# Performance work log

Hardware: AMD Instinct MI355X
Metric: run time of the kernel (lower is better)

The kernel has to match this reference:

```python
import jax, jax.numpy as jnp
import numpy as np

B, H, SEQLEN, HEAD_DIM = 1, 16, 4096, 64
SCALE = 1.0 / float(np.sqrt(HEAD_DIM))


def setup_inputs() -> dict:
    key = jax.random.key(0)
    kq, kk, kv = jax.random.split(key, 3)
    q = jax.random.normal(kq, (B, H, SEQLEN, HEAD_DIM), dtype=jnp.float32)
    k = jax.random.normal(kk, (B, H, HEAD_DIM, SEQLEN), dtype=jnp.float32)  # pre-transposed
    v = jax.random.normal(kv, (B, H, SEQLEN, HEAD_DIM), dtype=jnp.float32)
    return {"q": q, "k": k, "v": v}


def reference(q, k, v):
    # causal additive mask: -inf strictly above the diagonal
    mask = jnp.where(
        jnp.triu(jnp.ones((SEQLEN, SEQLEN), dtype=bool), k=1),
        jnp.float32(-jnp.inf), jnp.float32(0.0),
    ).astype(q.dtype)
    scores = jnp.einsum('bhsd,bhdt->bhst', q, k) * SCALE + mask  # [B,H,S,S]
    row_max = jnp.max(scores, axis=-1, keepdims=True)
    p_exp = jnp.exp(scores - row_max)
    denom = jnp.sum(p_exp, axis=-1, keepdims=True)
    p = p_exp / denom                                            # softmax probs
    out = jnp.einsum('bhst,bhtd->bhsd', p, v)                    # [B,H,S,D]
    row_sum = jnp.sum(p, axis=2)                                 # per-key accumulated attention [B,H,S]
    return (out, row_sum)
```

## Files before the change

kernel.cpp:

```cpp
#include <hip/hip_runtime.h>
#include <hip/hip_bf16.h>

#define HEADS 16
#define SEQ   4096
#define DIM   64
#define QT    64
#define KT    64
#define SCALE 0.125f
#define CF    0.18033688011112042f
#define LOG2E 1.4426950408889634f

typedef __bf16 v8bf  __attribute__((ext_vector_type(8)));
typedef __bf16 v4bf  __attribute__((ext_vector_type(4)));
typedef float  f32x4 __attribute__((ext_vector_type(4)));

__device__ __forceinline__ __bf16 to_bf(float f) { return (__bf16)f; }
__device__ __forceinline__ float ex2(float x) { return __builtin_amdgcn_exp2f(x); }
__device__ __forceinline__ float lg2(float x) { return __builtin_amdgcn_logf(x); }

__device__ __forceinline__ void gload16(const __bf16* g, __bf16* l) {
    __builtin_amdgcn_global_load_lds(
        (const __attribute__((address_space(1))) void*)g,
        (__attribute__((address_space(3))) void*)l,
        16, 0, 0);
}

__global__ __launch_bounds__(256) void conv_q_kernel(
    const float* __restrict__ qg, __bf16* __restrict__ Qb)
{
    size_t i = ((size_t)blockIdx.x * 256 + threadIdx.x) * 8;
    float4 f0 = *(const float4*)(qg + i);
    float4 f1 = *(const float4*)(qg + i + 4);
    v8bf o;
    o[0] = to_bf(f0.x * CF); o[1] = to_bf(f0.y * CF);
    o[2] = to_bf(f0.z * CF); o[3] = to_bf(f0.w * CF);
    o[4] = to_bf(f1.x * CF); o[5] = to_bf(f1.y * CF);
    o[6] = to_bf(f1.z * CF); o[7] = to_bf(f1.w * CF);
    *(v8bf*)(Qb + i) = o;
}

__global__ __launch_bounds__(256) void conv_kv_kernel(
    const float* __restrict__ kg, const float* __restrict__ vg,
    __bf16* __restrict__ Kb, __bf16* __restrict__ Vb)
{
    __shared__ __bf16 ldsT[64][65];
    const int h   = blockIdx.y;
    const int t0  = blockIdx.x * 64;
    const int tid = threadIdx.x;
    const int rr  = tid >> 2;
    const int cq  = (tid & 3) * 16;

    if (blockIdx.z == 0) {
        const float* src = kg + ((size_t)h * DIM + rr) * SEQ + t0 + cq;
        #pragma unroll
        for (int j = 0; j < 4; ++j) {
            float4 f = *(const float4*)(src + 4 * j);
            ldsT[rr][cq + 4 * j + 0] = to_bf(f.x);
            ldsT[rr][cq + 4 * j + 1] = to_bf(f.y);
            ldsT[rr][cq + 4 * j + 2] = to_bf(f.z);
            ldsT[rr][cq + 4 * j + 3] = to_bf(f.w);
        }
        __syncthreads();
        __bf16* dst = Kb + (size_t)h * SEQ * DIM + (size_t)(t0 + rr) * DIM + cq;
        v8bf o0, o1;
        #pragma unroll
        for (int i = 0; i < 8; ++i) {
            o0[i] = ldsT[cq + i][rr];
            o1[i] = ldsT[cq + 8 + i][rr];
        }
        *(v8bf*)dst = o0;
        *(v8bf*)(dst + 8) = o1;
    } else {
        const float* src = vg + ((size_t)h * SEQ + t0 + rr) * DIM + cq;
        #pragma unroll
        for (int j = 0; j < 4; ++j) {
            float4 f = *(const float4*)(src + 4 * j);
            ldsT[rr][cq + 4 * j + 0] = to_bf(f.x);
            ldsT[rr][cq + 4 * j + 1] = to_bf(f.y);
            ldsT[rr][cq + 4 * j + 2] = to_bf(f.z);
            ldsT[rr][cq + 4 * j + 3] = to_bf(f.w);
        }
        __syncthreads();
        __bf16* dst0 = Vb + ((size_t)h * DIM + rr) * SEQ + t0;
        const int n  = cq >> 4;
        const int c0 = 32 * (n >> 1) + 4 * (n & 1);
        #pragma unroll
        for (int j2 = 0; j2 < 4; ++j2) {
            v4bf ch;
            #pragma unroll
            for (int r = 0; r < 4; ++r)
                ch[r] = ldsT[cq + 4 * j2 + r][rr];
            *(v4bf*)(dst0 + c0 + 8 * j2) = ch;
        }
    }
}

__global__ __launch_bounds__(256, 2) void fa_fwd2_kernel(
    const __bf16* __restrict__ Qb, const __bf16* __restrict__ Kb,
    const __bf16* __restrict__ Vb, float* __restrict__ outg,
    float* __restrict__ lseg)
{
    const int b    = blockIdx.x;
    const int xcd  = b & 7;
    const int j    = b >> 3;
    const int h    = 2 * xcd + (j & 1);
    const int a    = j >> 1;
    const int tid  = threadIdx.x;
    const int wave = tid >> 6;
    const int lane = tid & 63;
    const int g    = lane >> 4;
    const int l16  = lane & 15;
    const int wit  = wave * 16 + l16;

    const int na  = a + 1;
    const int nb  = 64 - a;
    const int nIt = (nb + 1) >> 1;

    __shared__ alignas(16) __bf16 ldsK[2][2][KT * DIM];
    __shared__ alignas(16) __bf16 ldsV[2][2][DIM * KT];

    const int r0 = tid >> 3;
    const int c0 = tid & 7;
    const size_t kOff0 = (size_t)r0 * DIM + (size_t)((c0 ^ (r0 & 7)) << 3);
    const size_t kOff1 = (size_t)(r0 + 32) * DIM + (size_t)((c0 ^ ((r0 + 32) & 7)) << 3);
    const size_t vOff0 = (size_t)r0 * SEQ + (size_t)((c0 ^ (r0 & 7)) << 3);
    const size_t vOff1 = (size_t)(r0 + 32) * SEQ + (size_t)((c0 ^ ((r0 + 32) & 7)) << 3);
    const __bf16* KbH = Kb + (size_t)h * SEQ * DIM;
    const __bf16* VbH = Vb + (size_t)h * DIM * SEQ;
    const int ldsW = wave * 512;

    const int qlo = a * QT + wit;
    const int qhi = (63 - a) * QT + wit;

    const __bf16* qlr = Qb + ((size_t)h * SEQ + qlo) * DIM + g * 8;
    const __bf16* qhr = Qb + ((size_t)h * SEQ + qhi) * DIM + g * 8;
    v8bf aqlo0 = *(const v8bf*)qlr;
    v8bf aqlo1 = *(const v8bf*)(qlr + 32);
    v8bf aqhi0 = *(const v8bf*)qhr;
    v8bf aqhi1 = *(const v8bf*)(qhr + 32);

    f32x4 accl[4], acch[4];
    #pragma unroll
    for (int n = 0; n < 4; ++n) {
        accl[n] = (f32x4){0.f, 0.f, 0.f, 0.f};
        acch[n] = (f32x4){0.f, 0.f, 0.f, 0.f};
    }
    float lpl[4] = {0.f, 0.f, 0.f, 0.f};
    float lph[4] = {0.f, 0.f, 0.f, 0.f};

    int cur = 0;
    #pragma unroll
    for (int u = 0; u < 2; ++u) {
        const __bf16* kb = KbH + (size_t)(64 * u) * DIM;
        const __bf16* vb = VbH + 64 * u;
        gload16(kb + kOff0, &ldsK[0][u][ldsW]);
        gload16(kb + kOff1, &ldsK[0][u][2048 + ldsW]);
        gload16(vb + vOff0, &ldsV[0][u][ldsW]);
        gload16(vb + vOff1, &ldsV[0][u][2048 + ldsW]);
    }
    __syncthreads();

    auto sub_full = [&](int u, int t) {
        f32x4 sl[4], sh[4];
        #pragma unroll
        for (int n = 0; n < 4; ++n) {
            sl[n] = (f32x4){0.f, 0.f, 0.f, 0.f};
            sh[n] = (f32x4){0.f, 0.f, 0.f, 0.f};
        }
        __builtin_amdgcn_s_setprio(1);
        #pragma unroll
        for (int kk = 0; kk < 2; ++kk) {
            #pragma unroll
            for (int n = 0; n < 4; ++n) {
                int row  = 16 * n + l16;
                int byte = row * 128 + kk * 64 + g * 16;
                byte ^= (row & 7) << 4;
                v8bf ak = *(const v8bf*)&ldsK[cur][u][byte >> 1];
                sl[n] = __builtin_amdgcn_mfma_f32_16x16x32_bf16(
                    ak, kk ? aqlo1 : aqlo0, sl[n], 0, 0, 0);
                sh[n] = __builtin_amdgcn_mfma_f32_16x16x32_bf16(
                    ak, kk ? aqhi1 : aqhi0, sh[n], 0, 0, 0);
            }
        }
        __builtin_amdgcn_s_setprio(0);
        if (t >= na - 1) {
            const int lim = (a - t) * 64 + wit;
            #pragma unroll
            for (int n = 0; n < 4; ++n)
                #pragma unroll
                for (int r = 0; r < 4; ++r)
                    if (16 * n + 4 * g + r > lim) sl[n][r] = -3.0e38f;
        }
        v8bf pl0, pl1, ph0, ph1;
        #pragma unroll
        for (int n = 0; n < 4; ++n) {
            #pragma unroll
            for (int r = 0; r < 4; ++r) {
                float p = ex2(sl[n][r]);
                float q = ex2(sh[n][r]);
                lpl[r] += p;
                lph[r] += q;
                if (n < 2) { pl0[(n & 1) * 4 + r] = to_bf(p);
                             ph0[(n & 1) * 4 + r] = to_bf(q); }
                else       { pl1[(n & 1) * 4 + r] = to_bf(p);
                             ph1[(n & 1) * 4 + r] = to_bf(q); }
            }
        }
        __builtin_amdgcn_s_setprio(1);
        #pragma unroll
        for (int kk = 0; kk < 2; ++kk) {
            #pragma unroll
            for (int n = 0; n < 4; ++n) {
                int row  = 16 * n + l16;
                int byte = row * 128 + kk * 64 + g * 16;
                byte ^= (row & 7) << 4;
                v8bf av = *(const v8bf*)&ldsV[cur][u][byte >> 1];
                accl[n] = __builtin_amdgcn_mfma_f32_16x16x32_bf16(
                    av, kk ? pl1 : pl0, accl[n], 0, 0, 0);
                acch[n] = __builtin_amdgcn_mfma_f32_16x16x32_bf16(
                    av, kk ? ph1 : ph0, acch[n], 0, 0, 0);
            }
        }
        __builtin_amdgcn_s_setprio(0);
    };

    auto sub_hi = [&](int u, int t) {
        f32x4 sh[4];
        #pragma unroll
        for (int n = 0; n < 4; ++n) sh[n] = (f32x4){0.f, 0.f, 0.f, 0.f};
        __builtin_amdgcn_s_setprio(1);
        #pragma unroll
        for (int kk = 0; kk < 2; ++kk) {
            #pragma unroll
            for (int n = 0; n < 4; ++n) {
                int row  = 16 * n + l16;
                int byte = row * 128 + kk * 64 + g * 16;
                byte ^= (row & 7) << 4;
                v8bf ak = *(const v8bf*)&ldsK[cur][u][byte >> 1];
                sh[n] = __builtin_amdgcn_mfma_f32_16x16x32_bf16(
                    ak, kk ? aqhi1 : aqhi0, sh[n], 0, 0, 0);
            }
        }
        __builtin_amdgcn_s_setprio(0);
        if (t >= nb - 1) {
            const int lim = (63 - a - t) * 64 + wit;
            #pragma unroll
            for (int n = 0; n < 4; ++n)
                #pragma unroll
                for (int r = 0; r < 4; ++r)
                    if (16 * n + 4 * g + r > lim) sh[n][r] = -3.0e38f;
        }
        v8bf ph0, ph1;
        #pragma unroll
        for (int n = 0; n < 4; ++n) {
            #pragma unroll
            for (int r = 0; r < 4; ++r) {
                float q = ex2(sh[n][r]);
                lph[r] += q;
                if (n < 2) ph0[(n & 1) * 4 + r] = to_bf(q);
                else       ph1[(n & 1) * 4 + r] = to_bf(q);
            }
        }
        __builtin_amdgcn_s_setprio(1);
        #pragma unroll
        for (int kk = 0; kk < 2; ++kk) {
            #pragma unroll
            for (int n = 0; n < 4; ++n) {
                int row  = 16 * n + l16;
                int byte = row * 128 + kk * 64 + g * 16;
                byte ^= (row & 7) << 4;
                v8bf av = *(const v8bf*)&ldsV[cur][u][byte >> 1];
                acch[n] = __builtin_amdgcn_mfma_f32_16x16x32_bf16(
                    av, kk ? ph1 : ph0, acch[n], 0, 0, 0);
            }
        }
        __builtin_amdgcn_s_setprio(0);
    };

    #pragma unroll 1
    for (int it = 0; it < nIt; ++it) {
        if (it + 1 < nIt) {
            #pragma unroll
            for (int u = 0; u < 2; ++u) {
                const __bf16* kb = KbH + (size_t)(128 * (it + 1) + 64 * u) * DIM;
                const __bf16* vb = VbH + 128 * (it + 1) + 64 * u;
                gload16(kb + kOff0, &ldsK[cur ^ 1][u][ldsW]);
                gload16(kb + kOff1, &ldsK[cur ^ 1][u][2048 + ldsW]);
                gload16(vb + vOff0, &ldsV[cur ^ 1][u][ldsW]);
                gload16(vb + vOff1, &ldsV[cur ^ 1][u][2048 + ldsW]);
            }
        }
        const int t0 = 2 * it;
        if (t0 < na) { sub_full(0, t0); sub_full(1, t0 + 1); }
        else         { sub_hi(0, t0);   sub_hi(1, t0 + 1);   }
        __syncthreads();
        cur ^= 1;
    }

    {
        float l = (lpl[0] + lpl[1]) + (lpl[2] + lpl[3]);
        l += __shfl_xor(l, 16);
        l += __shfl_xor(l, 32);
        const float inv = 1.0f / l;
        float* orow = outg + ((size_t)h * SEQ + qlo) * DIM;
        #pragma unroll
        for (int n = 0; n < 4; ++n) {
            f32x4 o = accl[n];
            o[0] *= inv; o[1] *= inv; o[2] *= inv; o[3] *= inv;
            *(f32x4*)(orow + 16 * n + 4 * g) = o;
        }
        if (g == 0) lseg[h * SEQ + qlo] = lg2(l);
    }
    {
        float l = (lph[0] + lph[1]) + (lph[2] + lph[3]);
        l += __shfl_xor(l, 16);
        l += __shfl_xor(l, 32);
        const float inv = 1.0f / l;
        float* orow = outg + ((size_t)h * SEQ + qhi) * DIM;
        #pragma unroll
        for (int n = 0; n < 4; ++n) {
            f32x4 o = acch[n];
            o[0] *= inv; o[1] *= inv; o[2] *= inv; o[3] *= inv;
            *(f32x4*)(orow + 16 * n + 4 * g) = o;
        }
        if (g == 0) lseg[h * SEQ + qhi] = lg2(l);
    }
}

__global__ __launch_bounds__(256, 4) void fa_colsum2_kernel(
    const __bf16* __restrict__ Qb, const __bf16* __restrict__ Kb,
    const float* __restrict__ lseg, float* __restrict__ partg)
{
    const int b    = blockIdx.x;
    const int xcd  = b & 7;
    const int j    = b >> 3;
    const int h    = 2 * xcd + (j & 1);
    const int m    = j >> 1;
    const int ta   = m & 31;
    const int half = m >> 5;
    const int tb   = 63 - ta;
    const int smid = (ta <= 15) ? (ta + 33) : 48;
    const int qlo  = half ? smid : ta;
    const int qhiE = half ? 64 : smid;
    const int tid  = threadIdx.x;
    const int wave = tid >> 6;
    const int lane = tid & 63;
    const int g    = lane >> 4;
    const int l16  = lane & 15;

    __shared__ alignas(16) __bf16 ldsK2[2][KT * DIM];
    __shared__ float cs[2][4][KT];

    const int r0 = tid >> 3;
    const int c0 = tid & 7;
    const size_t kOff0 = (size_t)r0 * DIM + (size_t)((c0 ^ (r0 & 7)) << 3);
    const size_t kOff1 = (size_t)(r0 + 32) * DIM + (size_t)((c0 ^ ((r0 + 32) & 7)) << 3);
    const __bf16* KbH = Kb + (size_t)h * SEQ * DIM;
    const int ldsW = wave * 512;

    gload16(KbH + (size_t)ta * KT * DIM + kOff0, &ldsK2[0][ldsW]);
    gload16(KbH + (size_t)ta * KT * DIM + kOff1, &ldsK2[0][2048 + ldsW]);
    gload16(KbH + (size_t)tb * KT * DIM + kOff0, &ldsK2[1][ldsW]);
    gload16(KbH + (size_t)tb * KT * DIM + kOff1, &ldsK2[1][2048 + ldsW]);
    __syncthreads();

    float accA[4] = {0.f, 0.f, 0.f, 0.f};
    float accB[4] = {0.f, 0.f, 0.f, 0.f};

    #pragma unroll 1
    for (int qt = qlo; qt < qhiE; ++qt) {
        const int qw = qt * QT + wave * 16;
        const __bf16* qrow = Qb + ((size_t)h * SEQ + qw + l16) * DIM + g * 8;
        v8bf aq0 = *(const v8bf*)qrow;
        v8bf aq1 = *(const v8bf*)(qrow + 32);
        float4 lse4 = *(const float4*)(lseg + (size_t)h * SEQ + qw + 4 * g);

        {
            f32x4 s[4];
            #pragma unroll
            for (int n = 0; n < 4; ++n) s[n] = (f32x4){0.f, 0.f, 0.f, 0.f};
            __builtin_amdgcn_s_setprio(1);
            #pragma unroll
            for (int kk = 0; kk < 2; ++kk)
                #pragma unroll
                for (int n = 0; n < 4; ++n) {
                    int row  = 16 * n + l16;
                    int byte = row * 128 + kk * 64 + g * 16;
                    byte ^= (row & 7) << 4;
                    v8bf bk = *(const v8bf*)&ldsK2[0][byte >> 1];
                    s[n] = __builtin_amdgcn_mfma_f32_16x16x32_bf16(
                        kk ? aq1 : aq0, bk, s[n], 0, 0, 0);
                }
            __builtin_amdgcn_s_setprio(0);
            if (qt == ta) {
                #pragma unroll
                for (int n = 0; n < 4; ++n) {
                    const int key = ta * KT + 16 * n + l16;
                    #pragma unroll
                    for (int r = 0; r < 4; ++r) {
                        float e = ex2(s[n][r] - lse4[r]);
                        accA[n] += (key <= qw + 4 * g + r) ? e : 0.f;
                    }
                }
            } else {
                #pragma unroll
                for (int n = 0; n < 4; ++n)
                    #pragma unroll
                    for (int r = 0; r < 4; ++r)
                        accA[n] += ex2(s[n][r] - lse4[r]);
            }
        }
        if (qt >= tb) {
            f32x4 s[4];
            #pragma unroll
            for (int n = 0; n < 4; ++n) s[n] = (f32x4){0.f, 0.f, 0.f, 0.f};
            __builtin_amdgcn_s_setprio(1);
            #pragma unroll
            for (int kk = 0; kk < 2; ++kk)
                #pragma unroll
                for (int n = 0; n < 4; ++n) {
                    int row  = 16 * n + l16;
                    int byte = row * 128 + kk * 64 + g * 16;
                    byte ^= (row & 7) << 4;
                    v8bf bk = *(const v8bf*)&ldsK2[1][byte >> 1];
                    s[n] = __builtin_amdgcn_mfma_f32_16x16x32_bf16(
                        kk ? aq1 : aq0, bk, s[n], 0, 0, 0);
                }
            __builtin_amdgcn_s_setprio(0);
            if (qt == tb) {
                #pragma unroll
                for (int n = 0; n < 4; ++n) {
                    const int key = tb * KT + 16 * n + l16;
                    #pragma unroll
                    for (int r = 0; r < 4; ++r) {
                        float e = ex2(s[n][r] - lse4[r]);
                        accB[n] += (key <= qw + 4 * g + r) ? e : 0.f;
                    }
                }
            } else {
                #pragma unroll
                for (int n = 0; n < 4; ++n)
                    #pragma unroll
                    for (int r = 0; r < 4; ++r)
                        accB[n] += ex2(s[n][r] - lse4[r]);
            }
        }
    }

    #pragma unroll
    for (int n = 0; n < 4; ++n) {
        accA[n] += __shfl_xor(accA[n], 16);
        accA[n] += __shfl_xor(accA[n], 32);
        accB[n] += __shfl_xor(accB[n], 16);
        accB[n] += __shfl_xor(accB[n], 32);
    }
    if (lane < 16) {
        #pragma unroll
        for (int n = 0; n < 4; ++n) {
            cs[0][wave][16 * n + lane] = accA[n];
            cs[1][wave][16 * n + lane] = accB[n];
        }
    }
    __syncthreads();
    float* pg = partg + (size_t)half * HEADS * SEQ + (size_t)h * SEQ;
    if (tid < KT) {
        pg[ta * KT + tid] =
            cs[0][0][tid] + cs[0][1][tid] + cs[0][2][tid] + cs[0][3][tid];
    } else if (tid < 2 * KT) {
        const int t = tid - KT;
        pg[tb * KT + t] =
            cs[1][0][t] + cs[1][1][t] + cs[1][2][t] + cs[1][3][t];
    }
}

__global__ __launch_bounds__(256) void rs_add_kernel(
    const float* __restrict__ partg, float* __restrict__ rsg)
{
    const int i = blockIdx.x * 256 + threadIdx.x;
    f32x4 x = *(const f32x4*)(partg + (size_t)i * 4);
    f32x4 y = *(const f32x4*)(partg + (size_t)HEADS * SEQ + (size_t)i * 4);
    x[0] += y[0]; x[1] += y[1]; x[2] += y[2]; x[3] += y[3];
    *(f32x4*)(rsg + (size_t)i * 4) = x;
}

__global__ __launch_bounds__(256, 1) void fa_fwd_v1_kernel(
    const float* __restrict__ qg, const float* __restrict__ kg,
    const float* __restrict__ vg, float* __restrict__ outg,
    float* __restrict__ lseg)
{
    const int h    = blockIdx.y;
    const int q0   = blockIdx.x * QT;
    const int tid  = threadIdx.x;
    const int wave = tid >> 6;
    const int lane = tid & 63;
    const int g    = lane >> 4;
    const int l16  = lane & 15;

    __shared__ alignas(16) __bf16 ldsK[KT * DIM];
    __shared__ alignas(16) __bf16 ldsV[DIM * KT];
    __shared__ alignas(16) __bf16 ldsP[4][16 * 72];

    const int qw = q0 + wave * 16;
    v8bf aq[2];
    {
        const float* qrow = qg + ((size_t)h * SEQ + qw + l16) * DIM;
        #pragma unroll
        for (int kk = 0; kk < 2; ++kk) {
            const float* p = qrow + kk * 32 + g * 8;
            float4 f0 = *(const float4*)p;
            float4 f1 = *(const float4*)(p + 4);
            aq[kk][0] = to_bf(f0.x); aq[kk][1] = to_bf(f0.y);
            aq[kk][2] = to_bf(f0.z); aq[kk][3] = to_bf(f0.w);
            aq[kk][4] = to_bf(f1.x); aq[kk][5] = to_bf(f1.y);
            aq[kk][6] = to_bf(f1.z); aq[kk][7] = to_bf(f1.w);
        }
    }
    f32x4 acc[4];
    #pragma unroll
    for (int n = 0; n < 4; ++n) acc[n] = (f32x4){0.f, 0.f, 0.f, 0.f};
    float m_r[4], l_r[4];
    #pragma unroll
    for (int r = 0; r < 4; ++r) { m_r[r] = -__builtin_inff(); l_r[r] = 0.f; }

    const int ntiles = q0 / KT + 1;
    const int kd = tid >> 2;
    const int kc = (tid & 3) * 16;

    for (int t = 0; t < ntiles; ++t) {
        const int t0 = t * KT;
        __syncthreads();
        {
            const float* src = kg + ((size_t)h * DIM + kd) * SEQ + t0 + kc;
            #pragma unroll
            for (int j = 0; j < 4; ++j) {
                float4 f = *(const float4*)(src + 4 * j);
                #pragma unroll
                for (int i = 0; i < 4; ++i) {
                    int row  = kc + 4 * j + i;
                    int byte = row * 128 + kd * 2;
                    byte ^= (row & 7) << 4;
                    ldsK[byte >> 1] = to_bf(((const float*)&f)[i]);
                }
            }
        }
        {
            const float* src = vg + ((size_t)h * SEQ + t0 + kd) * DIM + kc;
            #pragma unroll
            for (int j = 0; j < 4; ++j) {
                float4 f = *(const float4*)(src + 4 * j);
                #pragma unroll
                for (int i = 0; i < 4; ++i) {
                    int row  = kc + 4 * j + i;
                    int byte = row * 128 + kd * 2;
                    byte ^= (row & 7) << 4;
                    ldsV[byte >> 1] = to_bf(((const float*)&f)[i]);
                }
            }
        }
        __syncthreads();

        f32x4 s[4];
        #pragma unroll
        for (int n = 0; n < 4; ++n) s[n] = (f32x4){0.f, 0.f, 0.f, 0.f};
        #pragma unroll
        for (int kk = 0; kk < 2; ++kk)
            #pragma unroll
            for (int n = 0; n < 4; ++n) {
                int row  = 16 * n + l16;
                int byte = row * 128 + kk * 64 + g * 16;
                byte ^= (row & 7) << 4;
                v8bf bk = *(const v8bf*)&ldsK[byte >> 1];
                s[n] = __builtin_amdgcn_mfma_f32_16x16x32_bf16(aq[kk], bk, s[n], 0, 0, 0);
            }
        float pvv[4][4];
        #pragma unroll
        for (int r = 0; r < 4; ++r) {
            const int qq = qw + 4 * g + r;
            float sv[4];
            #pragma unroll
            for (int n = 0; n < 4; ++n) {
                int key = t0 + 16 * n + l16;
                sv[n] = (key <= qq) ? s[n][r] * (SCALE * LOG2E) : -3.0e38f;
            }
            float mx = fmaxf(fmaxf(sv[0], sv[1]), fmaxf(sv[2], sv[3]));
            mx = fmaxf(mx, __shfl_xor(mx, 1));
            mx = fmaxf(mx, __shfl_xor(mx, 2));
            mx = fmaxf(mx, __shfl_xor(mx, 4));
            mx = fmaxf(mx, __shfl_xor(mx, 8));
            float mnew = fmaxf(m_r[r], mx);
            float corr = ex2(m_r[r] - mnew);
            m_r[r] = mnew;
            float rs = 0.f;
            #pragma unroll
            for (int n = 0; n < 4; ++n) {
                float p = (sv[n] > -1.0e38f) ? ex2(sv[n] - mnew) : 0.f;
                pvv[n][r] = p;
                rs += p;
            }
            rs += __shfl_xor(rs, 1);
            rs += __shfl_xor(rs, 2);
            rs += __shfl_xor(rs, 4);
            rs += __shfl_xor(rs, 8);
            l_r[r] = l_r[r] * corr + rs;
            #pragma unroll
            for (int n = 0; n < 4; ++n) acc[n][r] *= corr;
        }
        #pragma unroll
        for (int n = 0; n < 4; ++n)
            #pragma unroll
            for (int r = 0; r < 4; ++r)
                ldsP[wave][(4 * g + r) * 72 + 16 * n + l16] = to_bf(pvv[n][r]);
        asm volatile("s_waitcnt lgkmcnt(0)" ::: "memory");
        __builtin_amdgcn_sched_barrier(0);
        #pragma unroll
        for (int kk = 0; kk < 2; ++kk) {
            v8bf ap = *(const v8bf*)&ldsP[wave][l16 * 72 + 32 * kk + 8 * g];
            #pragma unroll
            for (int n = 0; n < 4; ++n) {
                int row  = 16 * n + l16;
                int byte = row * 128 + kk * 64 + g * 16;
                byte ^= (row & 7) << 4;
                v8bf bv = *(const v8bf*)&ldsV[byte >> 1];
                acc[n] = __builtin_amdgcn_mfma_f32_16x16x32_bf16(ap, bv, acc[n], 0, 0, 0);
            }
        }
    }
    #pragma unroll
    for (int r = 0; r < 4; ++r) {
        const int qq  = qw + 4 * g + r;
        const float inv = 1.0f / l_r[r];
        float* orow = outg + ((size_t)h * SEQ + qq) * DIM;
        #pragma unroll
        for (int n = 0; n < 4; ++n)
            orow[16 * n + l16] = acc[n][r] * inv;
        if (l16 == 0)
            lseg[h * SEQ + qq] = m_r[r] + lg2(l_r[r]);
    }
}

__global__ __launch_bounds__(256, 1) void fa_colsum_v1_kernel(
    const float* __restrict__ qg, const float* __restrict__ kg,
    const float* __restrict__ lseg, float* __restrict__ rsg)
{
    const int h    = blockIdx.y;
    const int t0   = blockIdx.x * KT;
    const int tid  = threadIdx.x;
    const int wave = tid >> 6;
    const int lane = tid & 63;
    const int g    = lane >> 4;
    const int l16  = lane & 15;

    __shared__ alignas(16) __bf16 ldsK[KT * DIM];
    __shared__ float cs[4][KT];
    {
        const int kd = tid >> 2;
        const int kc = (tid & 3) * 16;
        const float* src = kg + ((size_t)h * DIM + kd) * SEQ + t0 + kc;
        #pragma unroll
        for (int j = 0; j < 4; ++j) {
            float4 f = *(const float4*)(src + 4 * j);
            #pragma unroll
            for (int i = 0; i < 4; ++i) {
                int row  = kc + 4 * j + i;
                int byte = row * 128 + kd * 2;
                byte ^= (row & 7) << 4;
                ldsK[byte >> 1] = to_bf(((const float*)&f)[i]);
            }
        }
    }
    __syncthreads();
    float colacc[4] = {0.f, 0.f, 0.f, 0.f};
    for (int qt = t0 / QT; qt < SEQ / QT; ++qt) {
        const int qw = qt * QT + wave * 16;
        const float* qrow = qg + ((size_t)h * SEQ + qw + l16) * DIM;
        v8bf aq[2];
        #pragma unroll
        for (int kk = 0; kk < 2; ++kk) {
            const float* p = qrow + kk * 32 + g * 8;
            float4 f0 = *(const float4*)p;
            float4 f1 = *(const float4*)(p + 4);
            aq[kk][0] = to_bf(f0.x); aq[kk][1] = to_bf(f0.y);
            aq[kk][2] = to_bf(f0.z); aq[kk][3] = to_bf(f0.w);
            aq[kk][4] = to_bf(f1.x); aq[kk][5] = to_bf(f1.y);
            aq[kk][6] = to_bf(f1.z); aq[kk][7] = to_bf(f1.w);
        }
        float lse_r[4];
        #pragma unroll
        for (int r = 0; r < 4; ++r)
            lse_r[r] = lseg[h * SEQ + qw + 4 * g + r];
        f32x4 s[4];
        #pragma unroll
        for (int n = 0; n < 4; ++n) s[n] = (f32x4){0.f, 0.f, 0.f, 0.f};
        #pragma unroll
        for (int kk = 0; kk < 2; ++kk)
            #pragma unroll
            for (int n = 0; n < 4; ++n) {
                int row  = 16 * n + l16;
                int byte = row * 128 + kk * 64 + g * 16;
                byte ^= (row & 7) << 4;
                v8bf bk = *(const v8bf*)&ldsK[byte >> 1];
                s[n] = __builtin_amdgcn_mfma_f32_16x16x32_bf16(aq[kk], bk, s[n], 0, 0, 0);
            }
        #pragma unroll
        for (int n = 0; n < 4; ++n) {
            const int key = t0 + 16 * n + l16;
            #pragma unroll
            for (int r = 0; r < 4; ++r) {
                const int qq = qw + 4 * g + r;
                if (key <= qq)
                    colacc[n] += ex2(s[n][r] * (SCALE * LOG2E) - lse_r[r]);
            }
        }
    }
    #pragma unroll
    for (int n = 0; n < 4; ++n) {
        colacc[n] += __shfl_xor(colacc[n], 16);
        colacc[n] += __shfl_xor(colacc[n], 32);
    }
    if (lane < 16) {
        #pragma unroll
        for (int n = 0; n < 4; ++n)
            cs[wave][16 * n + lane] = colacc[n];
    }
    __syncthreads();
    if (tid < KT) {
        float v = cs[0][tid] + cs[1][tid] + cs[2][tid] + cs[3][tid];
        rsg[h * SEQ + t0 + tid] = v;
    }
}

extern "C" void kernel_launch(void* const* d_in, const int* in_sizes, int n_in,
                              void* d_out, int out_size, void* d_ws, size_t ws_size,
                              hipStream_t stream) {
    (void)in_sizes; (void)n_in; (void)out_size;
    const float* qg = (const float*)d_in[0];
    const float* kg = (const float*)d_in[1];
    const float* vg = (const float*)d_in[2];
    float* outg = (float*)d_out;
    float* rsg  = outg + (size_t)HEADS * SEQ * DIM;

    const size_t nElem   = (size_t)HEADS * SEQ * DIM;
    const size_t lseB    = (size_t)HEADS * SEQ * sizeof(float);
    const size_t needB   = lseB + 3 * nElem * sizeof(__bf16);

    if (ws_size >= needB) {
        float*  lseg = (float*)d_ws;
        __bf16* Qb = (__bf16*)((char*)d_ws + lseB);
        __bf16* Kb = Qb + nElem;
        __bf16* Vb = Kb + nElem;
        float* partg = (float*)Vb;
        conv_q_kernel<<<dim3((int)(nElem / 2048)), 256, 0, stream>>>(qg, Qb);
        conv_kv_kernel<<<dim3(SEQ / 64, HEADS, 2), 256, 0, stream>>>(kg, vg, Kb, Vb);
        fa_fwd2_kernel<<<dim3(512), 256, 0, stream>>>(Qb, Kb, Vb, outg, lseg);
        fa_colsum2_kernel<<<dim3(1024), 256, 0, stream>>>(Qb, Kb, lseg, partg);
        rs_add_kernel<<<dim3(HEADS * SEQ / 1024), 256, 0, stream>>>(partg, rsg);
    } else {
        float* lseg = (float*)d_ws;
        dim3 grid(SEQ / QT, HEADS);
        fa_fwd_v1_kernel<<<grid, 256, 0, stream>>>(qg, kg, vg, outg, lseg);
        fa_colsum_v1_kernel<<<grid, 256, 0, stream>>>(qg, kg, lseg, rsg);
    }
}
```

Before: 106.3 us.

## Fuse Q/K/V conversion kernels and drop split colsum with reduction pass

The Q conversion is merged into the K/V conversion kernel as a third z-slice, so one launch replaces two. The column-sum kernel no longer splits each key-tile pair's query range into two halves with partial buffers. It now runs 512 blocks, each looping over the full query range and writing row sums directly, which removes the rs_add kernel and the partial-buffer traffic. The trade-off is half as many colsum blocks, each with longer serial work, and launch bounds lowered to 2 blocks per CU, which may reduce parallelism and occupancy.

Result: faster. 99.99 us (-5.9%).

```diff
diff --git a/kernel.cpp b/kernel.cpp
--- a/kernel.cpp
+++ b/kernel.cpp
@@ -25,22 +25,9 @@
         16, 0, 0);
 }
 
-__global__ __launch_bounds__(256) void conv_q_kernel(
-    const float* __restrict__ qg, __bf16* __restrict__ Qb)
-{
-    size_t i = ((size_t)blockIdx.x * 256 + threadIdx.x) * 8;
-    float4 f0 = *(const float4*)(qg + i);
-    float4 f1 = *(const float4*)(qg + i + 4);
-    v8bf o;
-    o[0] = to_bf(f0.x * CF); o[1] = to_bf(f0.y * CF);
-    o[2] = to_bf(f0.z * CF); o[3] = to_bf(f0.w * CF);
-    o[4] = to_bf(f1.x * CF); o[5] = to_bf(f1.y * CF);
-    o[6] = to_bf(f1.z * CF); o[7] = to_bf(f1.w * CF);
-    *(v8bf*)(Qb + i) = o;
-}
-
-__global__ __launch_bounds__(256) void conv_kv_kernel(
-    const float* __restrict__ kg, const float* __restrict__ vg,
+__global__ __launch_bounds__(256) void conv_fused_kernel(
+    const float* __restrict__ qg, const float* __restrict__ kg,
+    const float* __restrict__ vg, __bf16* __restrict__ Qb,
     __bf16* __restrict__ Kb, __bf16* __restrict__ Vb)
 {
     __shared__ __bf16 ldsT[64][65];
@@ -49,6 +36,26 @@
     const int tid = threadIdx.x;
     const int rr  = tid >> 2;
     const int cq  = (tid & 3) * 16;
+
+    if (blockIdx.z == 2) {
+        const float* src = qg + ((size_t)h * SEQ + t0 + rr) * DIM + cq;
+        __bf16* dst = Qb + ((size_t)h * SEQ + t0 + rr) * DIM + cq;
+        v8bf o0, o1;
+        #pragma unroll
+        for (int j = 0; j < 2; ++j) {
+            float4 f0 = *(const float4*)(src + 8 * j);
+            float4 f1 = *(const float4*)(src + 8 * j + 4);
+            v8bf o;
+            o[0] = to_bf(f0.x * CF); o[1] = to_bf(f0.y * CF);
+            o[2] = to_bf(f0.z * CF); o[3] = to_bf(f0.w * CF);
+            o[4] = to_bf(f1.x * CF); o[5] = to_bf(f1.y * CF);
+            o[6] = to_bf(f1.z * CF); o[7] = to_bf(f1.w * CF);
+            if (j == 0) o0 = o; else o1 = o;
+        }
+        *(v8bf*)dst = o0;
+        *(v8bf*)(dst + 8) = o1;
+        return;
+    }
 
     if (blockIdx.z == 0) {
         const float* src = kg + ((size_t)h * DIM + rr) * SEQ + t0 + cq;
@@ -327,21 +334,16 @@
     }
 }
 
-__global__ __launch_bounds__(256, 4) void fa_colsum2_kernel(
+__global__ __launch_bounds__(256, 2) void fa_colsum2_kernel(
     const __bf16* __restrict__ Qb, const __bf16* __restrict__ Kb,
-    const float* __restrict__ lseg, float* __restrict__ partg)
+    const float* __restrict__ lseg, float* __restrict__ rsg)
 {
     const int b    = blockIdx.x;
     const int xcd  = b & 7;
     const int j    = b >> 3;
     const int h    = 2 * xcd + (j & 1);
-    const int m    = j >> 1;
-    const int ta   = m & 31;
-    const int half = m >> 5;
+    const int ta   = j >> 1;
     const int tb   = 63 - ta;
-    const int smid = (ta <= 15) ? (ta + 33) : 48;
-    const int qlo  = half ? smid : ta;
-    const int qhiE = half ? 64 : smid;
     const int tid  = threadIdx.x;
     const int wave = tid >> 6;
     const int lane = tid & 63;
@@ -368,7 +370,7 @@
     float accB[4] = {0.f, 0.f, 0.f, 0.f};
 
     #pragma unroll 1
-    for (int qt = qlo; qt < qhiE; ++qt) {
+    for (int qt = ta; qt < SEQ / QT; ++qt) {
         const int qw = qt * QT + wave * 16;
         const __bf16* qrow = Qb + ((size_t)h * SEQ + qw + l16) * DIM + g * 8;
         v8bf aq0 = *(const v8bf*)qrow;
@@ -462,25 +464,14 @@
         }
     }
     __syncthreads();
-    float* pg = partg + (size_t)half * HEADS * SEQ + (size_t)h * SEQ;
     if (tid < KT) {
-        pg[ta * KT + tid] =
+        rsg[(size_t)h * SEQ + ta * KT + tid] =
             cs[0][0][tid] + cs[0][1][tid] + cs[0][2][tid] + cs[0][3][tid];
     } else if (tid < 2 * KT) {
         const int t = tid - KT;
-        pg[tb * KT + t] =
+        rsg[(size_t)h * SEQ + tb * KT + t] =
             cs[1][0][t] + cs[1][1][t] + cs[1][2][t] + cs[1][3][t];
     }
-}
-
-__global__ __launch_bounds__(256) void rs_add_kernel(
-    const float* __restrict__ partg, float* __restrict__ rsg)
-{
-    const int i = blockIdx.x * 256 + threadIdx.x;
-    f32x4 x = *(const f32x4*)(partg + (size_t)i * 4);
-    f32x4 y = *(const f32x4*)(partg + (size_t)HEADS * SEQ + (size_t)i * 4);
-    x[0] += y[0]; x[1] += y[1]; x[2] += y[2]; x[3] += y[3];
-    *(f32x4*)(rsg + (size_t)i * 4) = x;
 }
 
 __global__ __launch_bounds__(256, 1) void fa_fwd_v1_kernel(
@@ -748,12 +739,10 @@
         __bf16* Qb = (__bf16*)((char*)d_ws + lseB);
         __bf16* Kb = Qb + nElem;
         __bf16* Vb = Kb + nElem;
-        float* partg = (float*)Vb;
-        conv_q_kernel<<<dim3((int)(nElem / 2048)), 256, 0, stream>>>(qg, Qb);
-        conv_kv_kernel<<<dim3(SEQ / 64, HEADS, 2), 256, 0, stream>>>(kg, vg, Kb, Vb);
+        conv_fused_kernel<<<dim3(SEQ / 64, HEADS, 3), 256, 0, stream>>>(
+            qg, kg, vg, Qb, Kb, Vb);
         fa_fwd2_kernel<<<dim3(512), 256, 0, stream>>>(Qb, Kb, Vb, outg, lseg);
-        fa_colsum2_kernel<<<dim3(1024), 256, 0, stream>>>(Qb, Kb, lseg, partg);
-        rs_add_kernel<<<dim3(HEADS * SEQ / 1024), 256, 0, stream>>>(partg, rsg);
+        fa_colsum2_kernel<<<dim3(512), 256, 0, stream>>>(Qb, Kb, lseg, rsg);
     } else {
         float* lseg = (float*)d_ws;
         dim3 grid(SEQ / QT, HEADS);
```
